# Kernel tuning notes

Hardware: AMD Instinct MI355X
Metric: run time of the kernel (lower is better)

## Reference

```python
import jax, jax.numpy as jnp
import numpy as np

N_NODES = 50000
N_EDGES = 800000
D = 64


def setup_inputs() -> dict:
    key = jax.random.key(0)
    k1, k2, k3, k4, k5 = jax.random.split(key, 5)
    graph_embedding = jax.random.normal(k1, (N_NODES, D), dtype=jnp.float32)
    weight = jax.random.normal(k2, (1, D), dtype=jnp.float32)  # xavier-like scale not critical
    src = jax.random.randint(k3, (N_EDGES,), 0, N_NODES, dtype=jnp.int32)
    dst = jax.random.randint(k4, (N_EDGES,), 0, N_NODES, dtype=jnp.int32)
    e_feat = jax.random.randint(k5, (N_EDGES,), 0, 6, dtype=jnp.int32)
    return {"graph_embedding": graph_embedding, "weight": weight,
            "src": src, "dst": dst, "e_feat": e_feat}


def reference(graph_embedding, weight, src, dst, e_feat):
    n_nodes = graph_embedding.shape[0]
    # emb == ft == ft0 == ft3 == ft4 == ft5 in the original module
    emb = jax.nn.elu(graph_embedding * weight)  # [N, D]
    e = e_feat  # integer edge-type codes; original float cast + == gives same result
    # two-hop message: ft + [e==0]*ft0 + [e==4]*ft4 + [e==5]*ft5, all equal to emb[src]
    scale = (1.0 + (e == 0).astype(emb.dtype)
                 + (e == 4).astype(emb.dtype)
                 + (e == 5).astype(emb.dtype))  # [E]
    msg2 = emb[src] * scale[:, None]  # [E, D]
    ft_twohop = jax.ops.segment_sum(msg2, dst, num_segments=n_nodes)  # [N, D]
    # one-hop message: select two-hop feature of source on edges of type 3
    msg1 = jnp.where((e == 3)[:, None], ft_twohop[src], jnp.zeros((), emb.dtype))  # [E, D]
    res = jax.ops.segment_sum(msg1, dst, num_segments=n_nodes)  # [N, D]
    return res
```

## Files before the change

kernel.cpp:

```cpp
#include <hip/hip_runtime.h>

#define D 64
#define CAP 48
#define CAP3 16
#define NBW 256
#define QW 32
#define EPB 2048
#define CELL 40
#define SEGSTRIDE 4608

__device__ __forceinline__ unsigned short f2bf(float f) {
    union { float f; unsigned u; } v; v.f = f;
    unsigned r = (v.u + 0x7FFFu + ((v.u >> 16) & 1u)) >> 16;
    return (unsigned short)r;
}
__device__ __forceinline__ float bf2f(unsigned short h) {
    union { unsigned u; float f; } v; v.u = ((unsigned)h) << 16;
    return v.f;
}

__global__ __launch_bounds__(256) void k_combo(
        const int* __restrict__ src, const int* __restrict__ dst, const int* __restrict__ ef,
        unsigned* __restrict__ seg, int* __restrict__ segcnt,
        const float4* __restrict__ g4, const float4* __restrict__ w4,
        unsigned short* __restrict__ embb,
        int n_edges, int nb, int nblkA, int n_elems) {
    __shared__ unsigned lcell[256 * CELL];
    __shared__ int lcnt[256];
    int tid = threadIdx.x;

    if (blockIdx.x < (unsigned)nblkA) {
        int base = blockIdx.x * EPB;
        lcnt[tid] = 0;
        __syncthreads();

        int e0 = base + tid * 8;
        if (e0 + 8 <= n_edges) {
            int4 d0 = *(const int4*)(dst + e0), d1 = *(const int4*)(dst + e0 + 4);
            int4 s0 = *(const int4*)(src + e0), s1 = *(const int4*)(src + e0 + 4);
            int4 f0 = *(const int4*)(ef  + e0), f1 = *(const int4*)(ef  + e0 + 4);
            int ds[8] = {d0.x, d0.y, d0.z, d0.w, d1.x, d1.y, d1.z, d1.w};
            int ss[8] = {s0.x, s0.y, s0.z, s0.w, s1.x, s1.y, s1.z, s1.w};
            int fs[8] = {f0.x, f0.y, f0.z, f0.w, f1.x, f1.y, f1.z, f1.w};
            #pragma unroll
            for (int j = 0; j < 8; ++j) {
                int b = ds[j] >> 8;
                unsigned rec = (unsigned)ss[j] | ((unsigned)fs[j] << 16)
                             | ((unsigned)(ds[j] & 255) << 19);
                int pos = atomicAdd(&lcnt[b], 1);
                if (pos < CELL) lcell[b * CELL + pos] = rec;
            }
        } else {
            for (int j = 0; j < 8; ++j) {
                int e = e0 + j;
                if (e < n_edges) {
                    int d = dst[e];
                    unsigned rec = (unsigned)src[e] | ((unsigned)ef[e] << 16)
                                 | ((unsigned)(d & 255) << 19);
                    int pos = atomicAdd(&lcnt[d >> 8], 1);
                    if (pos < CELL) lcell[(d >> 8) * CELL + pos] = rec;
                }
            }
        }
        __syncthreads();

        if (tid < nb) {
            int v = lcnt[tid]; if (v > CELL) v = CELL;
            if (v > 0) {
                int off = atomicAdd(&segcnt[tid], v);
                unsigned* dstp = seg + (size_t)tid * SEGSTRIDE + off;
                for (int k = 0; k < v; ++k) dstp[k] = lcell[tid * CELL + k];
            }
        }
    } else {
        int i = (blockIdx.x - nblkA) * 256 + tid;
        if (i * 8 >= n_elems) return;
        float4 a = g4[i * 2];
        float4 b = g4[i * 2 + 1];
        float4 wa = w4[(i * 2) & 15];
        float4 wb = w4[(i * 2 + 1) & 15];
        a.x *= wa.x; a.y *= wa.y; a.z *= wa.z; a.w *= wa.w;
        b.x *= wb.x; b.y *= wb.y; b.z *= wb.z; b.w *= wb.w;
        a.x = a.x > 0.f ? a.x : (expf(a.x) - 1.f);
        a.y = a.y > 0.f ? a.y : (expf(a.y) - 1.f);
        a.z = a.z > 0.f ? a.z : (expf(a.z) - 1.f);
        a.w = a.w > 0.f ? a.w : (expf(a.w) - 1.f);
        b.x = b.x > 0.f ? b.x : (expf(b.x) - 1.f);
        b.y = b.y > 0.f ? b.y : (expf(b.y) - 1.f);
        b.z = b.z > 0.f ? b.z : (expf(b.z) - 1.f);
        b.w = b.w > 0.f ? b.w : (expf(b.w) - 1.f);
        uint4 o;
        o.x = (unsigned)f2bf(a.x) | ((unsigned)f2bf(a.y) << 16);
        o.y = (unsigned)f2bf(a.z) | ((unsigned)f2bf(a.w) << 16);
        o.z = (unsigned)f2bf(b.x) | ((unsigned)f2bf(b.y) << 16);
        o.w = (unsigned)f2bf(b.z) | ((unsigned)f2bf(b.w) << 16);
        *(uint4*)(embb + (size_t)i * 8) = o;
    }
}

__global__ __launch_bounds__(256) void k_fuse(
        const unsigned short* __restrict__ embb,
        const unsigned* __restrict__ seg, const int* __restrict__ segcnt,
        unsigned short* __restrict__ ftb, int* __restrict__ cnt3, unsigned* __restrict__ ell3,
        int nb, int n_nodes) {
    __shared__ unsigned lpay[QW * CAP];
    __shared__ unsigned lpay3[QW * CAP3];
    __shared__ int lc[QW];
    __shared__ int lc3[QW];
    int bucket = blockIdx.x >> 3;
    int q      = blockIdx.x & 7;
    int lo     = bucket * NBW + q * QW;
    int tid = threadIdx.x;
    int wave = tid >> 6, lane = tid & 63;
    for (int i = tid; i < QW; i += 256) { lc[i] = 0; lc3[i] = 0; }
    __syncthreads();

    int total = segcnt[bucket];
    if (total > SEGSTRIDE) total = SEGSTRIDE;
    const unsigned* segp = seg + (size_t)bucket * SEGSTRIDE;
    int total4 = total & ~3;
    for (int i = tid * 4; i < total4; i += 256 * 4) {
        uint4 rv = *(const uint4*)(segp + i);
        unsigned rs[4] = {rv.x, rv.y, rv.z, rv.w};
        #pragma unroll
        for (int k = 0; k < 4; ++k) {
            unsigned rec = rs[k];
            unsigned r = rec >> 19;
            if ((int)(r >> 5) == q) {
                unsigned rr = r & 31;
                unsigned pl = rec & 0x7FFFFu;
                int pos = atomicAdd(&lc[rr], 1);
                if (pos < CAP) lpay[rr * CAP + pos] = pl;
                if (((rec >> 16) & 7u) == 3u) {
                    int p3 = atomicAdd(&lc3[rr], 1);
                    if (p3 < CAP3) lpay3[rr * CAP3 + p3] = pl;
                }
            }
        }
    }
    if (tid < (total - total4)) {
        unsigned rec = segp[total4 + tid];
        unsigned r = rec >> 19;
        if ((int)(r >> 5) == q) {
            unsigned rr = r & 31;
            unsigned pl = rec & 0x7FFFFu;
            int pos = atomicAdd(&lc[rr], 1);
            if (pos < CAP) lpay[rr * CAP + pos] = pl;
            if (((rec >> 16) & 7u) == 3u) {
                int p3 = atomicAdd(&lc3[rr], 1);
                if (p3 < CAP3) lpay3[rr * CAP3 + p3] = pl;
            }
        }
    }
    __syncthreads();

    int grp = lane >> 4;
    int dq  = (lane & 15) * 4;
    #pragma unroll 2
    for (int n = wave; n < QW; n += 4) {
        int node = lo + n;
        if (node >= n_nodes) break;
        int deg = lc[n]; deg = deg < CAP ? deg : CAP;
        const unsigned* row = lpay + n * CAP;
        float4 acc = {0.f, 0.f, 0.f, 0.f};
        for (int base = 0; base < deg; base += 16) {
            int e0 = base + grp, e1 = e0 + 4, e2 = e0 + 8, e3 = e0 + 12;
            if (e0 < deg) {
                unsigned p = row[e0]; int et = p >> 16;
                float s = 1.f + (float)(et == 0) + (float)(et == 4) + (float)(et == 5);
                ushort4 u = *(const ushort4*)(embb + (size_t)(p & 0xFFFF) * D + dq);
                acc.x += bf2f(u.x) * s; acc.y += bf2f(u.y) * s;
                acc.z += bf2f(u.z) * s; acc.w += bf2f(u.w) * s;
            }
            if (e1 < deg) {
                unsigned p = row[e1]; int et = p >> 16;
                float s = 1.f + (float)(et == 0) + (float)(et == 4) + (float)(et == 5);
                ushort4 u = *(const ushort4*)(embb + (size_t)(p & 0xFFFF) * D + dq);
                acc.x += bf2f(u.x) * s; acc.y += bf2f(u.y) * s;
                acc.z += bf2f(u.z) * s; acc.w += bf2f(u.w) * s;
            }
            if (e2 < deg) {
                unsigned p = row[e2]; int et = p >> 16;
                float s = 1.f + (float)(et == 0) + (float)(et == 4) + (float)(et == 5);
                ushort4 u = *(const ushort4*)(embb + (size_t)(p & 0xFFFF) * D + dq);
                acc.x += bf2f(u.x) * s; acc.y += bf2f(u.y) * s;
                acc.z += bf2f(u.z) * s; acc.w += bf2f(u.w) * s;
            }
            if (e3 < deg) {
                unsigned p = row[e3]; int et = p >> 16;
                float s = 1.f + (float)(et == 0) + (float)(et == 4) + (float)(et == 5);
                ushort4 u = *(const ushort4*)(embb + (size_t)(p & 0xFFFF) * D + dq);
                acc.x += bf2f(u.x) * s; acc.y += bf2f(u.y) * s;
                acc.z += bf2f(u.z) * s; acc.w += bf2f(u.w) * s;
            }
        }
        acc.x += __shfl_xor(acc.x, 16); acc.y += __shfl_xor(acc.y, 16);
        acc.z += __shfl_xor(acc.z, 16); acc.w += __shfl_xor(acc.w, 16);
        acc.x += __shfl_xor(acc.x, 32); acc.y += __shfl_xor(acc.y, 32);
        acc.z += __shfl_xor(acc.z, 32); acc.w += __shfl_xor(acc.w, 32);
        if (grp == 0) {
            ushort4 o;
            o.x = f2bf(acc.x); o.y = f2bf(acc.y); o.z = f2bf(acc.z); o.w = f2bf(acc.w);
            *(ushort4*)(ftb + (size_t)node * D + dq) = o;
        }
        if (lane < CAP3) ell3[(size_t)node * CAP3 + lane] = lpay3[n * CAP3 + lane];
        if (lane == 0) cnt3[node] = lc3[n] < CAP3 ? lc3[n] : CAP3;
    }
}

__global__ void k_onehop_gather(const unsigned short* __restrict__ ftb,
                                const int* __restrict__ cnt3,
                                const unsigned* __restrict__ ell3,
                                float* __restrict__ out, int n_nodes) {
    int gid  = blockIdx.x * blockDim.x + threadIdx.x;
    int node = gid >> 6;
    int lane = gid & 63;
    if (node >= n_nodes) return;
    int deg = cnt3[node];
    const unsigned* row = ell3 + (size_t)node * CAP3;
    int grp = lane >> 4;
    int dq  = (lane & 15) * 4;
    float acc0 = 0.f, acc1 = 0.f, acc2 = 0.f, acc3 = 0.f;
    for (int e = grp; e < deg; e += 4) {
        int i = row[e] & 0xFFFF;
        ushort4 u = *(const ushort4*)(ftb + (size_t)i * D + dq);
        acc0 += bf2f(u.x); acc1 += bf2f(u.y);
        acc2 += bf2f(u.z); acc3 += bf2f(u.w);
    }
    acc0 += __shfl_xor(acc0, 16); acc1 += __shfl_xor(acc1, 16);
    acc2 += __shfl_xor(acc2, 16); acc3 += __shfl_xor(acc3, 16);
    acc0 += __shfl_xor(acc0, 32); acc1 += __shfl_xor(acc1, 32);
    acc2 += __shfl_xor(acc2, 32); acc3 += __shfl_xor(acc3, 32);
    if (grp == 0) {
        float4 o = {acc0, acc1, acc2, acc3};
        *(float4*)(out + (size_t)node * D + dq) = o;
    }
}

extern "C" void kernel_launch(void* const* d_in, const int* in_sizes, int n_in,
                              void* d_out, int out_size, void* d_ws, size_t ws_size,
                              hipStream_t stream) {
    const float* g   = (const float*)d_in[0];
    const float* w   = (const float*)d_in[1];
    const int*   src = (const int*)d_in[2];
    const int*   dst = (const int*)d_in[3];
    const int*   ef  = (const int*)d_in[4];
    float* out = (float*)d_out;

    int n_elems = in_sizes[0];
    int n_nodes = n_elems / D;
    int n_edges = in_sizes[2];
    int nblkA   = (n_edges + EPB - 1) / EPB;
    int nb      = (n_nodes + NBW - 1) / NBW;

    unsigned short* embb   = (unsigned short*)d_ws;
    unsigned short* ftb    = embb + n_elems;
    int*            cnt3   = (int*)(ftb + n_elems);
    int*            segcnt = cnt3 + n_nodes + 64;
    unsigned*       ell3   = (unsigned*)(segcnt + nb + 64);
    unsigned*       seg    = ell3 + (size_t)n_nodes * CAP3;

    hipMemsetAsync(segcnt, 0, (size_t)nb * sizeof(int), stream);

    {
        int embBlocks = (n_elems / 8 + 255) / 256;
        k_combo<<<nblkA + embBlocks, 256, 0, stream>>>(
            src, dst, ef, seg, segcnt,
            (const float4*)g, (const float4*)w, embb,
            n_edges, nb, nblkA, n_elems);
    }
    k_fuse<<<nb * 8, 256, 0, stream>>>(embb, seg, segcnt, ftb, cnt3, ell3,
                                       nb, n_nodes);
    {
        long long total = (long long)n_nodes * D;
        int blocks = (int)((total + 255) / 256);
        k_onehop_gather<<<blocks, 256, 0, stream>>>(ftb, cnt3, ell3, out, n_nodes);
    }
}
```

Measured before the change: 126.8 us.

## Split bf16 embedding into two feature-half planes and gather each in a separate pass

The bf16 embedding table is stored as two planes, each holding 32 features per node. The two-hop fuse kernel now runs twice, once per plane, so each gather pass touches a table half the size. The intent is to shrink the random-gather working set so it fits better in L2/MALL. The cost is a second launch that re-reads and re-buckets the segment lists, and each gather now reads only 4 bytes per lane.

```diff
diff --git a/kernel.cpp b/kernel.cpp
--- a/kernel.cpp
+++ b/kernel.cpp
@@ -14,6 +14,12 @@
     unsigned r = (v.u + 0x7FFFu + ((v.u >> 16) & 1u)) >> 16;
     return (unsigned short)r;
 }
+__device__ __forceinline__ float bflo(unsigned u) {
+    union { unsigned x; float f; } v; v.x = u << 16; return v.f;
+}
+__device__ __forceinline__ float bfhi(unsigned u) {
+    union { unsigned x; float f; } v; v.x = u & 0xFFFF0000u; return v.f;
+}
 __device__ __forceinline__ float bf2f(unsigned short h) {
     union { unsigned u; float f; } v; v.u = ((unsigned)h) << 16;
     return v.f;
@@ -24,7 +30,7 @@
         unsigned* __restrict__ seg, int* __restrict__ segcnt,
         const float4* __restrict__ g4, const float4* __restrict__ w4,
         unsigned short* __restrict__ embb,
-        int n_edges, int nb, int nblkA, int n_elems) {
+        int n_edges, int nb, int nblkA, int n_elems, int n_nodes) {
     __shared__ unsigned lcell[256 * CELL];
     __shared__ int lcnt[256];
     int tid = threadIdx.x;
@@ -94,7 +100,11 @@
         o.y = (unsigned)f2bf(a.z) | ((unsigned)f2bf(a.w) << 16);
         o.z = (unsigned)f2bf(b.x) | ((unsigned)f2bf(b.y) << 16);
         o.w = (unsigned)f2bf(b.z) | ((unsigned)f2bf(b.w) << 16);
-        *(uint4*)(embb + (size_t)i * 8) = o;
+        int n  = (i * 8) >> 6;
+        int d0 = (i * 8) & 63;
+        int plane = d0 >> 5;
+        int off   = d0 & 31;
+        *(uint4*)(embb + (size_t)plane * (size_t)n_nodes * 32 + (size_t)n * 32 + off) = o;
     }
 }
 
@@ -102,7 +112,7 @@
         const unsigned short* __restrict__ embb,
         const unsigned* __restrict__ seg, const int* __restrict__ segcnt,
         unsigned short* __restrict__ ftb, int* __restrict__ cnt3, unsigned* __restrict__ ell3,
-        int nb, int n_nodes) {
+        int nb, int n_nodes, int plane) {
     __shared__ unsigned lpay[QW * CAP];
     __shared__ unsigned lpay3[QW * CAP3];
     __shared__ int lc[QW];
@@ -154,57 +164,53 @@
     }
     __syncthreads();
 
+    const unsigned short* embp = embb + (size_t)plane * (size_t)n_nodes * 32;
     int grp = lane >> 4;
-    int dq  = (lane & 15) * 4;
+    int dl  = lane & 15;
     #pragma unroll 2
     for (int n = wave; n < QW; n += 4) {
         int node = lo + n;
         if (node >= n_nodes) break;
         int deg = lc[n]; deg = deg < CAP ? deg : CAP;
         const unsigned* row = lpay + n * CAP;
-        float4 acc = {0.f, 0.f, 0.f, 0.f};
+        float accx = 0.f, accy = 0.f;
         for (int base = 0; base < deg; base += 16) {
             int e0 = base + grp, e1 = e0 + 4, e2 = e0 + 8, e3 = e0 + 12;
             if (e0 < deg) {
                 unsigned p = row[e0]; int et = p >> 16;
                 float s = 1.f + (float)(et == 0) + (float)(et == 4) + (float)(et == 5);
-                ushort4 u = *(const ushort4*)(embb + (size_t)(p & 0xFFFF) * D + dq);
-                acc.x += bf2f(u.x) * s; acc.y += bf2f(u.y) * s;
-                acc.z += bf2f(u.z) * s; acc.w += bf2f(u.w) * s;
+                unsigned u = *(const unsigned*)(embp + (size_t)(p & 0xFFFF) * 32 + dl * 2);
+                accx += bflo(u) * s; accy += bfhi(u) * s;
             }
             if (e1 < deg) {
                 unsigned p = row[e1]; int et = p >> 16;
                 float s = 1.f + (float)(et == 0) + (float)(et == 4) + (float)(et == 5);
-                ushort4 u = *(const ushort4*)(embb + (size_t)(p & 0xFFFF) * D + dq);
-                acc.x += bf2f(u.x) * s; acc.y += bf2f(u.y) * s;
-                acc.z += bf2f(u.z) * s; acc.w += bf2f(u.w) * s;
+                unsigned u = *(const unsigned*)(embp + (size_t)(p & 0xFFFF) * 32 + dl * 2);
+                accx += bflo(u) * s; accy += bfhi(u) * s;
             }
             if (e2 < deg) {
                 unsigned p = row[e2]; int et = p >> 16;
                 float s = 1.f + (float)(et == 0) + (float)(et == 4) + (float)(et == 5);
-                ushort4 u = *(const ushort4*)(embb + (size_t)(p & 0xFFFF) * D + dq);
-                acc.x += bf2f(u.x) * s; acc.y += bf2f(u.y) * s;
-                acc.z += bf2f(u.z) * s; acc.w += bf2f(u.w) * s;
+                unsigned u = *(const unsigned*)(embp + (size_t)(p & 0xFFFF) * 32 + dl * 2);
+                accx += bflo(u) * s; accy += bfhi(u) * s;
             }
             if (e3 < deg) {
                 unsigned p = row[e3]; int et = p >> 16;
                 float s = 1.f + (float)(et == 0) + (float)(et == 4) + (float)(et == 5);
-                ushort4 u = *(const ushort4*)(embb + (size_t)(p & 0xFFFF) * D + dq);
-                acc.x += bf2f(u.x) * s; acc.y += bf2f(u.y) * s;
-                acc.z += bf2f(u.z) * s; acc.w += bf2f(u.w) * s;
-            }
-        }
-        acc.x += __shfl_xor(acc.x, 16); acc.y += __shfl_xor(acc.y, 16);
-        acc.z += __shfl_xor(acc.z, 16); acc.w += __shfl_xor(acc.w, 16);
-        acc.x += __shfl_xor(acc.x, 32); acc.y += __shfl_xor(acc.y, 32);
-        acc.z += __shfl_xor(acc.z, 32); acc.w += __shfl_xor(acc.w, 32);
+                unsigned u = *(const unsigned*)(embp + (size_t)(p & 0xFFFF) * 32 + dl * 2);
+                accx += bflo(u) * s; accy += bfhi(u) * s;
+            }
+        }
+        accx += __shfl_xor(accx, 16); accy += __shfl_xor(accy, 16);
+        accx += __shfl_xor(accx, 32); accy += __shfl_xor(accy, 32);
         if (grp == 0) {
-            ushort4 o;
-            o.x = f2bf(acc.x); o.y = f2bf(acc.y); o.z = f2bf(acc.z); o.w = f2bf(acc.w);
-            *(ushort4*)(ftb + (size_t)node * D + dq) = o;
-        }
-        if (lane < CAP3) ell3[(size_t)node * CAP3 + lane] = lpay3[n * CAP3 + lane];
-        if (lane == 0) cnt3[node] = lc3[n] < CAP3 ? lc3[n] : CAP3;
+            unsigned o = (unsigned)f2bf(accx) | ((unsigned)f2bf(accy) << 16);
+            *(unsigned*)(ftb + (size_t)node * D + plane * 32 + dl * 2) = o;
+        }
+        if (plane == 0) {
+            if (lane < CAP3) ell3[(size_t)node * CAP3 + lane] = lpay3[n * CAP3 + lane];
+            if (lane == 0) cnt3[node] = lc3[n] < CAP3 ? lc3[n] : CAP3;
+        }
     }
 }
 
@@ -267,10 +273,12 @@
         k_combo<<<nblkA + embBlocks, 256, 0, stream>>>(
             src, dst, ef, seg, segcnt,
             (const float4*)g, (const float4*)w, embb,
-            n_edges, nb, nblkA, n_elems);
+            n_edges, nb, nblkA, n_elems, n_nodes);
     }
     k_fuse<<<nb * 8, 256, 0, stream>>>(embb, seg, segcnt, ftb, cnt3, ell3,
-                                       nb, n_nodes);
+                                       nb, n_nodes, 0);
+    k_fuse<<<nb * 8, 256, 0, stream>>>(embb, seg, segcnt, ftb, cnt3, ell3,
+                                       nb, n_nodes, 1);
     {
         long long total = (long long)n_nodes * D;
         int blocks = (int)((total + 255) / 256);
```

Result: slower. 148.5 us (+17.1%).
